# Kernel tuning notes

Hardware: AMD Instinct MI355X
Metric: run time of the kernel (lower is better)

The kernel has to match this reference:

```python
import jax, jax.numpy as jnp
import numpy as np
from jax import lax

SIGMA = 3.0
AP_CUT = 15


def _gauss_kernel(sigma, truncate=4.0):
    r = int(truncate * sigma + 0.5)
    x = np.arange(-r, r + 1, dtype=np.float32)
    k = np.exp(-0.5 * (x / sigma) ** 2)
    return jnp.asarray(k / k.sum()), r

KERN, RAD = _gauss_kernel(SIGMA)


def _smooth(f):
    """Separable Gaussian smoothing; circular on y (DV), replicate on x (AP).
    f: [..., Y, X] -> same shape."""
    lead = f.shape[:-2]
    Y, X = f.shape[-2:]
    g = f.reshape((-1, 1, Y, X))
    g = jnp.pad(g, ((0, 0), (0, 0), (RAD, RAD), (0, 0)), mode='wrap')
    g = jnp.pad(g, ((0, 0), (0, 0), (0, 0), (RAD, RAD)), mode='edge')
    ky = KERN.reshape(1, 1, -1, 1)
    kx = KERN.reshape(1, 1, 1, -1)
    g = lax.conv_general_dilated(g, ky, (1, 1), 'VALID')
    g = lax.conv_general_dilated(g, kx, (1, 1), 'VALID')
    return g.reshape(lead + (Y, X))


def _gradient(f):
    """Covariant gradient: Gaussian smooth then central differences.
    Returns [..., Y, X, 2] with index 0 = d/dy (circular), 1 = d/dx (replicate)."""
    g = _smooth(f)
    dy = 0.5 * (jnp.roll(g, -1, axis=-2) - jnp.roll(g, 1, axis=-2))
    gp = jnp.pad(g, [(0, 0)] * (g.ndim - 1) + [(1, 1)], mode='edge')
    dx = 0.5 * (gp[..., 2:] - gp[..., :-2])
    return jnp.stack([dy, dx], axis=-1)


def _postprocess(f):
    f = f.at[..., :AP_CUT].set(0.0)
    f = f.at[..., -AP_CUT:].set(0.0)
    return _smooth(f)


def setup_inputs() -> dict:
    key = jax.random.key(0)
    k1, k2 = jax.random.split(key)
    Y, X = 1024, 2048
    y = 0.1 * jax.random.normal(k1, (5, Y, X), dtype=jnp.float32)
    v = 0.1 * jax.random.normal(k2, (2, Y, X), dtype=jnp.float32)
    return {"y": y, "v": v}


def reference(y, v):
    Y, X = y.shape[-2:]
    # InputProcessor.transform: split state into 2x2 tensor m and scalar s
    m = y[:4].reshape(2, 2, Y, X)
    s = y[4]

    # get_velocity: left-right symmetrization (flip DV axis, negate y-component)
    v_lr = jnp.flip(v, axis=-2)
    v_lr = v_lr.at[0].multiply(-1.0)
    v = 0.5 * (v + v_lr)

    d1_m = _gradient(m)          # [2,2,Y,X,2]
    d1_s = _gradient(s)          # [Y,X,2]
    d1_v = _gradient(v)          # [2,Y,X,2]

    sdot = -jnp.einsum('iyx,yxi->yx', v, d1_s)

    T = jnp.transpose(d1_v, (0, 3, 1, 2))       # iyxj -> ijyx
    Tt = jnp.transpose(T, (1, 0, 2, 3))
    O = -0.5 * (T - Tt)                         # vorticity
    E = 0.5 * (T + Tt)                          # strain rate

    lhs = jnp.einsum('kyx,ijyxk->ijyx', v, d1_m)
    lhs = lhs + jnp.einsum('ikyx,kjyx->ijyx', O, m)
    lhs = lhs - jnp.einsum('ikyx,kjyx->ijyx', m, O)

    # rhs_eCad reaction terms
    trm = jnp.einsum('kkyx->yx', m)
    trE = jnp.einsum('kkyx->yx', E)
    gamma_dv = jnp.array([[1.0, 0.0], [0.0, 0.0]], dtype=y.dtype)[..., None, None]
    rhs = -(0.11 - 0.099 * s) * m
    rhs = rhs + (0.767 + 0.055 * s) * m * trE
    rhs = rhs + (0.732 - 0.59 * s) * trm * m
    rhs = rhs + (0.069 - 0.048 * s) * trm * gamma_dv

    mdot = _postprocess(-lhs + rhs)
    sdot = _postprocess(sdot)

    # inverse_transform: stack back into 5-channel state derivative
    return jnp.concatenate([mdot.reshape(4, Y, X), sdot[None]], axis=0)
```

## Files before the change

### kernel.cpp

```cpp
#include <hip/hip_runtime.h>
#include <math.h>

#define Y_ 1024
#define X_ 2048
#define YX_ (Y_*X_)
#define RAD_ 12
#define NT_ 25
#define APC_ 15
#define PAD_ 16

struct W25 { float w[NT_]; };

__device__ __forceinline__ void load9(float wb[36], const float* p) {
#pragma unroll
  for (int i = 0; i < 9; ++i) {
    float4 t = *(const float4*)(p + 4 * i);
    wb[4*i+0] = t.x; wb[4*i+1] = t.y; wb[4*i+2] = t.z; wb[4*i+3] = t.w;
  }
}

__device__ __forceinline__ void derivs_ch(
    const float* __restrict__ base, int yy, int yu, int yd, int x0,
    const W25& W, float dX[4], float dY[4])
{
  float wb[36];
  load9(wb, base + yy * X_ + x0 - 16);
  float wc6[6];
#pragma unroll
  for (int jj = 0; jj < 6; ++jj) {
    float s = 0.f;
#pragma unroll
    for (int t = 0; t < NT_; ++t) s += W.w[t] * wb[3 + jj + t];
    wc6[jj] = s;
  }
#pragma unroll
  for (int j = 0; j < 4; ++j) dX[j] = 0.5f * (wc6[j + 2] - wc6[j]);

  float au[4], ad[4];
  load9(wb, base + yu * X_ + x0 - 16);
#pragma unroll
  for (int j = 0; j < 4; ++j) {
    float s = 0.f;
#pragma unroll
    for (int t = 0; t < NT_; ++t) s += W.w[t] * wb[4 + j + t];
    au[j] = s;
  }
  load9(wb, base + yd * X_ + x0 - 16);
#pragma unroll
  for (int j = 0; j < 4; ++j) {
    float s = 0.f;
#pragma unroll
    for (int t = 0; t < NT_; ++t) s += W.w[t] * wb[4 + j + t];
    ad[j] = s;
  }
#pragma unroll
  for (int j = 0; j < 4; ++j) dY[j] = 0.5f * (au[j] - ad[j]);
}

__global__ __launch_bounds__(256) void ksmooth_y7c(
    const float* __restrict__ yin, const float* __restrict__ vin,
    float* __restrict__ out, W25 W)
{
  const int id = blockIdx.x;
  const int w  = (id & 7) * 112 + (id >> 3);
  const int yg = w % 64, xh = (w / 64) & 1, z = w / 128;
  const int y0 = yg * 16;
  const int xo = xh * 1024 + threadIdx.x * 4;

  float4 acc[16];
#pragma unroll
  for (int j = 0; j < 16; ++j) acc[j] = make_float4(0.f, 0.f, 0.f, 0.f);

  if (z < 5) {
    const float* base = yin + z * YX_;
#pragma unroll
    for (int g = 0; g < 4; ++g) {
      float4 b[10];
#pragma unroll
      for (int i = 0; i < 10; ++i) {
        const int r = (y0 - RAD_ + 10*g + i + Y_) & (Y_ - 1);
        b[i] = *(const float4*)(base + r * X_ + xo);
      }
#pragma unroll
      for (int i = 0; i < 10; ++i) {
        const int t = 10*g + i;
#pragma unroll
        for (int j = 0; j < 16; ++j) {
          const int k = t - j;
          if (k >= 0 && k < NT_) {
            const float wk = W.w[k];
            acc[j].x += wk * b[i].x; acc[j].y += wk * b[i].y;
            acc[j].z += wk * b[i].z; acc[j].w += wk * b[i].w;
          }
        }
      }
    }
  } else {
    const int   c   = z - 5;
    const float sgn = (c == 0) ? -1.f : 1.f;
    const float* base = vin + c * YX_;
#pragma unroll
    for (int g = 0; g < 8; ++g) {
      float4 a5[5], b5[5];
#pragma unroll
      for (int i = 0; i < 5; ++i) {
        const int r = (y0 - RAD_ + 5*g + i + Y_) & (Y_ - 1);
        a5[i] = *(const float4*)(base + r * X_ + xo);
        b5[i] = *(const float4*)(base + (Y_ - 1 - r) * X_ + xo);
      }
#pragma unroll
      for (int i = 0; i < 5; ++i) {
        const int t = 5*g + i;
        float4 val;
        val.x = 0.5f * (a5[i].x + sgn * b5[i].x);
        val.y = 0.5f * (a5[i].y + sgn * b5[i].y);
        val.z = 0.5f * (a5[i].z + sgn * b5[i].z);
        val.w = 0.5f * (a5[i].w + sgn * b5[i].w);
#pragma unroll
        for (int j = 0; j < 16; ++j) {
          const int k = t - j;
          if (k >= 0 && k < NT_) {
            const float wk = W.w[k];
            acc[j].x += wk * val.x; acc[j].y += wk * val.y;
            acc[j].z += wk * val.z; acc[j].w += wk * val.w;
          }
        }
      }
    }
  }
#pragma unroll
  for (int j = 0; j < 16; ++j)
    *(float4*)(out + z * YX_ + (y0 + j) * X_ + xo) = acc[j];
}

__global__ __launch_bounds__(256) void kfused(
    const float* __restrict__ gY,
    const float* __restrict__ yin,
    const float* __restrict__ vin,
    float* __restrict__ B,
    W25 W)
{
  const int id = blockIdx.x;
  const int w  = (id & 7) * 256 + (id >> 3);
  const int yy = w & (Y_ - 1);
  const int xh = w >> 10;
  const int x0 = xh * 1024 + threadIdx.x * 4;

  if (x0 < RAD_ || x0 > X_ - PAD_) {
#pragma unroll
    for (int zc = 0; zc < 5; ++zc)
      *(float4*)(B + zc * YX_ + yy * X_ + x0) = make_float4(0.f,0.f,0.f,0.f);
    return;
  }

  const int yu = (yy + 1) & (Y_ - 1);
  const int yd = (yy - 1) & (Y_ - 1);

  float v0[4], v1[4];
  {
    float4 a = *(const float4*)(vin + 0 * YX_ + yy * X_ + x0);
    float4 b = *(const float4*)(vin + 0 * YX_ + (Y_ - 1 - yy) * X_ + x0);
    float4 c = *(const float4*)(vin + 1 * YX_ + yy * X_ + x0);
    float4 d = *(const float4*)(vin + 1 * YX_ + (Y_ - 1 - yy) * X_ + x0);
    v0[0] = 0.5f*(a.x-b.x); v0[1] = 0.5f*(a.y-b.y);
    v0[2] = 0.5f*(a.z-b.z); v0[3] = 0.5f*(a.w-b.w);
    v1[0] = 0.5f*(c.x+d.x); v1[1] = 0.5f*(c.y+d.y);
    v1[2] = 0.5f*(c.z+d.z); v1[3] = 0.5f*(c.w+d.w);
  }

  float w_[4], trE[4];
  {
    float dX5[4], dY5[4], dX6[4], dY6[4];
    derivs_ch(gY + 5 * YX_, yy, yu, yd, x0, W, dX5, dY5);
    derivs_ch(gY + 6 * YX_, yy, yu, yd, x0, W, dX6, dY6);
#pragma unroll
    for (int j = 0; j < 4; ++j) {
      w_[j]  = -0.5f * (dX5[j] - dY6[j]);
      trE[j] = dY5[j] + dX6[j];
    }
  }

  float acc[5][4];
#pragma unroll
  for (int c = 0; c < 5; ++c) {
    float dX[4], dY[4];
    derivs_ch(gY + c * YX_, yy, yu, yd, x0, W, dX, dY);
#pragma unroll
    for (int j = 0; j < 4; ++j) acc[c][j] = v0[j] * dY[j] + v1[j] * dX[j];
  }

  float rm[5][4];
#pragma unroll
  for (int zc = 0; zc < 5; ++zc) {
    float4 t = *(const float4*)(yin + zc * YX_ + yy * X_ + x0);
    rm[zc][0] = t.x; rm[zc][1] = t.y; rm[zc][2] = t.z; rm[zc][3] = t.w;
  }

  float o[5][4];
#pragma unroll
  for (int j = 0; j < 4; ++j) {
    const float m00r = rm[0][j], m01r = rm[1][j], m10r = rm[2][j], m11r = rm[3][j];
    const float sr   = rm[4][j];
    const float wj   = w_[j];
    const float trm  = m00r + m11r;

    const float lhs00 = acc[0][j] + wj * (m10r + m01r);
    const float lhs01 = acc[1][j] + wj * (m11r - m00r);
    const float lhs10 = acc[2][j] + wj * (m11r - m00r);
    const float lhs11 = acc[3][j] - wj * (m01r + m10r);

    const float f  = -(0.11f - 0.099f * sr)
                   + (0.767f + 0.055f * sr) * trE[j]
                   + (0.732f - 0.59f  * sr) * trm;
    const float cd = (0.069f - 0.048f * sr) * trm;
    const float sd = -acc[4][j];

    const int   xg   = x0 + j;
    const float mask = (xg < APC_ || xg >= X_ - APC_) ? 0.f : 1.f;
    o[0][j] = mask * (f * m00r + cd - lhs00);
    o[1][j] = mask * (f * m01r      - lhs01);
    o[2][j] = mask * (f * m10r      - lhs10);
    o[3][j] = mask * (f * m11r      - lhs11);
    o[4][j] = mask * sd;
  }
#pragma unroll
  for (int zc = 0; zc < 5; ++zc)
    *(float4*)(B + zc * YX_ + yy * X_ + x0) =
        make_float4(o[zc][0], o[zc][1], o[zc][2], o[zc][3]);
}

__global__ __launch_bounds__(256) void kxsmooth(
    const float* __restrict__ in, float* __restrict__ out, W25 W)
{
  const int z  = blockIdx.z;
  const int yy = blockIdx.y;
  const int x0 = (blockIdx.x * 256 + threadIdx.x) * 4;
  const float* row = in + z * YX_ + yy * X_;

  float buf[28];
  if (x0 >= RAD_ && x0 + 4 + RAD_ <= X_) {
#pragma unroll
    for (int i = 0; i < 7; ++i) {
      float4 t = *(const float4*)(row + x0 - RAD_ + 4 * i);
      buf[4*i+0] = t.x; buf[4*i+1] = t.y; buf[4*i+2] = t.z; buf[4*i+3] = t.w;
    }
  } else {
#pragma unroll
    for (int i = 0; i < 28; ++i) {
      int xx = x0 - RAD_ + i;
      xx = xx < 0 ? 0 : (xx > X_ - 1 ? X_ - 1 : xx);
      buf[i] = row[xx];
    }
  }
  float a0 = 0.f, a1 = 0.f, a2 = 0.f, a3 = 0.f;
#pragma unroll
  for (int t = 0; t < NT_; ++t) {
    const float wk = W.w[t];
    a0 += wk * buf[t + 0];
    a1 += wk * buf[t + 1];
    a2 += wk * buf[t + 2];
    a3 += wk * buf[t + 3];
  }
  *(float4*)(out + z * YX_ + yy * X_ + x0) = make_float4(a0, a1, a2, a3);
}

__global__ __launch_bounds__(256) void ksmooth_y5c(
    const float* __restrict__ in, float* __restrict__ out, W25 W)
{
  const int id = blockIdx.x;
  const int w  = (id & 7) * 80 + (id >> 3);
  const int yg = w % 64, xh = (w / 64) & 1, z = w / 128;
  const int y0 = yg * 16;
  const int xo = xh * 1024 + threadIdx.x * 4;
  const float* base = in + z * YX_;

  float4 acc[16];
#pragma unroll
  for (int j = 0; j < 16; ++j) acc[j] = make_float4(0.f, 0.f, 0.f, 0.f);

#pragma unroll
  for (int g = 0; g < 4; ++g) {
    float4 b[10];
#pragma unroll
    for (int i = 0; i < 10; ++i) {
      const int r = (y0 - RAD_ + 10*g + i + Y_) & (Y_ - 1);
      b[i] = *(const float4*)(base + r * X_ + xo);
    }
#pragma unroll
    for (int i = 0; i < 10; ++i) {
      const int t = 10*g + i;
#pragma unroll
      for (int j = 0; j < 16; ++j) {
        const int k = t - j;
        if (k >= 0 && k < NT_) {
          const float wk = W.w[k];
          acc[j].x += wk * b[i].x; acc[j].y += wk * b[i].y;
          acc[j].z += wk * b[i].z; acc[j].w += wk * b[i].w;
        }
      }
    }
  }
#pragma unroll
  for (int j = 0; j < 16; ++j)
    *(float4*)(out + z * YX_ + (y0 + j) * X_ + xo) = acc[j];
}

extern "C" void kernel_launch(void* const* d_in, const int* in_sizes, int n_in,
                              void* d_out, int out_size, void* d_ws, size_t ws_size,
                              hipStream_t stream)
{
  const float* yin = (const float*)d_in[0];
  const float* vin = (const float*)d_in[1];
  float* out = (float*)d_out;

  float* gY = (float*)d_ws + PAD_;
  float* B  = gY + 7 * (size_t)YX_;
  float* C  = gY;

  W25 W;
  double wd[NT_], s = 0.0;
  for (int i = 0; i < NT_; ++i) {
    const double x = i - RAD_;
    wd[i] = exp(-0.5 * (x / 3.0) * (x / 3.0));
    s += wd[i];
  }
  for (int i = 0; i < NT_; ++i) W.w[i] = (float)(wd[i] / s);

  ksmooth_y7c<<<896,  256, 0, stream>>>(yin, vin, gY, W);
  kfused     <<<2048, 256, 0, stream>>>(gY, yin, vin, B, W);
  kxsmooth   <<<dim3(2, 1024, 5), 256, 0, stream>>>(B, C, W);
  ksmooth_y5c<<<640,  256, 0, stream>>>(C, out, W);
}
```

Measured before the change: 224.3 us.

## Stage gradient rows in LDS with double buffering and fused derivative taps

The fused gradient kernel now stages the three needed rows of each y-smoothed channel into shared memory once per block, double-buffered across the seven channels. Neighbouring threads then read the overlapping x-stencil from LDS instead of issuing redundant global float4 loads. The x-derivative folds the smoothing and central difference into one precomputed 27-tap kernel, and the y-derivative differences the rows before convolving, which roughly halves the multiply-adds. The edge-block early exit is removed, so boundary threads now run the full computation and rely on the mask plus padding to read in bounds. In exchange the kernel adds a __syncthreads per channel and LDS use that may limit occupancy.

```diff
diff --git a/kernel.cpp b/kernel.cpp
--- a/kernel.cpp
+++ b/kernel.cpp
@@ -6,56 +6,12 @@
 #define YX_ (Y_*X_)
 #define RAD_ 12
 #define NT_ 25
+#define ND_ 27
 #define APC_ 15
 #define PAD_ 16
 
 struct W25 { float w[NT_]; };
-
-__device__ __forceinline__ void load9(float wb[36], const float* p) {
-#pragma unroll
-  for (int i = 0; i < 9; ++i) {
-    float4 t = *(const float4*)(p + 4 * i);
-    wb[4*i+0] = t.x; wb[4*i+1] = t.y; wb[4*i+2] = t.z; wb[4*i+3] = t.w;
-  }
-}
-
-__device__ __forceinline__ void derivs_ch(
-    const float* __restrict__ base, int yy, int yu, int yd, int x0,
-    const W25& W, float dX[4], float dY[4])
-{
-  float wb[36];
-  load9(wb, base + yy * X_ + x0 - 16);
-  float wc6[6];
-#pragma unroll
-  for (int jj = 0; jj < 6; ++jj) {
-    float s = 0.f;
-#pragma unroll
-    for (int t = 0; t < NT_; ++t) s += W.w[t] * wb[3 + jj + t];
-    wc6[jj] = s;
-  }
-#pragma unroll
-  for (int j = 0; j < 4; ++j) dX[j] = 0.5f * (wc6[j + 2] - wc6[j]);
-
-  float au[4], ad[4];
-  load9(wb, base + yu * X_ + x0 - 16);
-#pragma unroll
-  for (int j = 0; j < 4; ++j) {
-    float s = 0.f;
-#pragma unroll
-    for (int t = 0; t < NT_; ++t) s += W.w[t] * wb[4 + j + t];
-    au[j] = s;
-  }
-  load9(wb, base + yd * X_ + x0 - 16);
-#pragma unroll
-  for (int j = 0; j < 4; ++j) {
-    float s = 0.f;
-#pragma unroll
-    for (int t = 0; t < NT_; ++t) s += W.w[t] * wb[4 + j + t];
-    ad[j] = s;
-  }
-#pragma unroll
-  for (int j = 0; j < 4; ++j) dY[j] = 0.5f * (au[j] - ad[j]);
-}
+struct D27 { float d[ND_]; };
 
 __global__ __launch_bounds__(256) void ksmooth_y7c(
     const float* __restrict__ yin, const float* __restrict__ vin,
@@ -133,28 +89,63 @@
     *(float4*)(out + z * YX_ + (y0 + j) * X_ + xo) = acc[j];
 }
 
-__global__ __launch_bounds__(256) void kfused(
+__device__ __forceinline__ void stage_row(
+    float (&slot)[4][264], const float* __restrict__ src, int tid)
+{
+  float4 v = *(const float4*)(src + 4 * tid);
+  slot[0][tid] = v.x; slot[1][tid] = v.y; slot[2][tid] = v.z; slot[3][tid] = v.w;
+  if (tid < 8) {
+    float4 v2 = *(const float4*)(src + 1024 + 4 * tid);
+    slot[0][256+tid] = v2.x; slot[1][256+tid] = v2.y;
+    slot[2][256+tid] = v2.z; slot[3][256+tid] = v2.w;
+  }
+}
+
+__device__ __forceinline__ void conv_lds(
+    const float (&L)[3][4][264], int tid, const W25& W, const D27& D,
+    float dX[4], float dY[4])
+{
+#pragma unroll
+  for (int j = 0; j < 4; ++j) { dX[j] = 0.f; dY[j] = 0.f; }
+#pragma unroll
+  for (int i = 3; i <= 33; ++i) {
+    const float v = L[1][i & 3][tid + (i >> 2)];
+#pragma unroll
+    for (int j = 0; j < 4; ++j) {
+      const int k = i - 3 - j;
+      if (k >= 0 && k < ND_) dX[j] += D.d[k] * v;
+    }
+  }
+#pragma unroll
+  for (int i = 4; i <= 31; ++i) {
+    const float u = L[2][i & 3][tid + (i >> 2)];
+    const float d = L[0][i & 3][tid + (i >> 2)];
+    const float dv = 0.5f * (u - d);
+#pragma unroll
+    for (int j = 0; j < 4; ++j) {
+      const int k = i - 4 - j;
+      if (k >= 0 && k < NT_) dY[j] += W.w[k] * dv;
+    }
+  }
+}
+
+__global__ __launch_bounds__(256) void kfused_lds(
     const float* __restrict__ gY,
     const float* __restrict__ yin,
     const float* __restrict__ vin,
     float* __restrict__ B,
-    W25 W)
-{
-  const int id = blockIdx.x;
-  const int w  = (id & 7) * 256 + (id >> 3);
-  const int yy = w & (Y_ - 1);
-  const int xh = w >> 10;
-  const int x0 = xh * 1024 + threadIdx.x * 4;
-
-  if (x0 < RAD_ || x0 > X_ - PAD_) {
-#pragma unroll
-    for (int zc = 0; zc < 5; ++zc)
-      *(float4*)(B + zc * YX_ + yy * X_ + x0) = make_float4(0.f,0.f,0.f,0.f);
-    return;
-  }
-
-  const int yu = (yy + 1) & (Y_ - 1);
-  const int yd = (yy - 1) & (Y_ - 1);
+    W25 W, D27 D)
+{
+  __shared__ float lds[2][3][4][264];
+  const int tid = threadIdx.x;
+  const int id  = blockIdx.x;
+  const int w   = (id & 7) * 256 + (id >> 3);
+  const int yy  = w & (Y_ - 1);
+  const int xh  = w >> 10;
+  const int xb  = xh * 1024;
+  const int x0  = xb + 4 * tid;
+  const int yu  = (yy + 1) & (Y_ - 1);
+  const int yd  = (yy - 1) & (Y_ - 1);
 
   float v0[4], v1[4];
   {
@@ -168,25 +159,50 @@
     v1[2] = 0.5f*(c.z+d.z); v1[3] = 0.5f*(c.w+d.w);
   }
 
-  float w_[4], trE[4];
+  float dXa[4], dYa[4], w_[4], trE[4];
+  float ac0[4], ac1[4], ac2[4], ac3[4], ac4[4];
+
   {
-    float dX5[4], dY5[4], dX6[4], dY6[4];
-    derivs_ch(gY + 5 * YX_, yy, yu, yd, x0, W, dX5, dY5);
-    derivs_ch(gY + 6 * YX_, yy, yu, yd, x0, W, dX6, dY6);
-#pragma unroll
-    for (int j = 0; j < 4; ++j) {
-      w_[j]  = -0.5f * (dX5[j] - dY6[j]);
-      trE[j] = dY5[j] + dX6[j];
-    }
-  }
-
-  float acc[5][4];
-#pragma unroll
-  for (int c = 0; c < 5; ++c) {
+    const float* b5 = gY + 5 * YX_;
+    stage_row(lds[0][0], b5 + yd * X_ + xb - 16, tid);
+    stage_row(lds[0][1], b5 + yy * X_ + xb - 16, tid);
+    stage_row(lds[0][2], b5 + yu * X_ + xb - 16, tid);
+  }
+  __syncthreads();
+
+#pragma unroll
+  for (int ci = 0; ci < 7; ++ci) {
+    if (ci < 6) {
+      const int nch = (ci == 0) ? 6 : ci - 1;
+      const float* bn = gY + nch * YX_;
+      const int nb = (ci + 1) & 1;
+      stage_row(lds[nb][0], bn + yd * X_ + xb - 16, tid);
+      stage_row(lds[nb][1], bn + yy * X_ + xb - 16, tid);
+      stage_row(lds[nb][2], bn + yu * X_ + xb - 16, tid);
+    }
     float dX[4], dY[4];
-    derivs_ch(gY + c * YX_, yy, yu, yd, x0, W, dX, dY);
-#pragma unroll
-    for (int j = 0; j < 4; ++j) acc[c][j] = v0[j] * dY[j] + v1[j] * dX[j];
+    conv_lds(lds[ci & 1], tid, W, D, dX, dY);
+    if (ci == 0) {
+#pragma unroll
+      for (int j = 0; j < 4; ++j) { dXa[j] = dX[j]; dYa[j] = dY[j]; }
+    } else if (ci == 1) {
+#pragma unroll
+      for (int j = 0; j < 4; ++j) {
+        w_[j]  = -0.5f * (dXa[j] - dY[j]);
+        trE[j] = dYa[j] + dX[j];
+      }
+    } else {
+#pragma unroll
+      for (int j = 0; j < 4; ++j) {
+        const float t = v0[j] * dY[j] + v1[j] * dX[j];
+        if (ci == 2) ac0[j] = t;
+        if (ci == 3) ac1[j] = t;
+        if (ci == 4) ac2[j] = t;
+        if (ci == 5) ac3[j] = t;
+        if (ci == 6) ac4[j] = t;
+      }
+    }
+    __syncthreads();
   }
 
   float rm[5][4];
@@ -204,16 +220,16 @@
     const float wj   = w_[j];
     const float trm  = m00r + m11r;
 
-    const float lhs00 = acc[0][j] + wj * (m10r + m01r);
-    const float lhs01 = acc[1][j] + wj * (m11r - m00r);
-    const float lhs10 = acc[2][j] + wj * (m11r - m00r);
-    const float lhs11 = acc[3][j] - wj * (m01r + m10r);
+    const float lhs00 = ac0[j] + wj * (m10r + m01r);
+    const float lhs01 = ac1[j] + wj * (m11r - m00r);
+    const float lhs10 = ac2[j] + wj * (m11r - m00r);
+    const float lhs11 = ac3[j] - wj * (m01r + m10r);
 
     const float f  = -(0.11f - 0.099f * sr)
                    + (0.767f + 0.055f * sr) * trE[j]
                    + (0.732f - 0.59f  * sr) * trm;
     const float cd = (0.069f - 0.048f * sr) * trm;
-    const float sd = -acc[4][j];
+    const float sd = -ac4[j];
 
     const int   xg   = x0 + j;
     const float mask = (xg < APC_ || xg >= X_ - APC_) ? 0.f : 1.f;
@@ -317,7 +333,7 @@
   float* B  = gY + 7 * (size_t)YX_;
   float* C  = gY;
 
-  W25 W;
+  W25 W; D27 D;
   double wd[NT_], s = 0.0;
   for (int i = 0; i < NT_; ++i) {
     const double x = i - RAD_;
@@ -325,9 +341,14 @@
     s += wd[i];
   }
   for (int i = 0; i < NT_; ++i) W.w[i] = (float)(wd[i] / s);
+  for (int t = 0; t < ND_; ++t) {
+    const double a = (t - 2 >= 0 && t - 2 < NT_) ? wd[t - 2] / s : 0.0;
+    const double b = (t < NT_) ? wd[t] / s : 0.0;
+    D.d[t] = (float)(0.5 * (a - b));
+  }
 
   ksmooth_y7c<<<896,  256, 0, stream>>>(yin, vin, gY, W);
-  kfused     <<<2048, 256, 0, stream>>>(gY, yin, vin, B, W);
+  kfused_lds <<<2048, 256, 0, stream>>>(gY, yin, vin, B, W, D);
   kxsmooth   <<<dim3(2, 1024, 5), 256, 0, stream>>>(B, C, W);
   ksmooth_y5c<<<640,  256, 0, stream>>>(C, out, W);
 }
```

New measurement: 324.2 us. 44.5% more time.
